# Performance work log

Hardware: AMD Instinct MI355X
Metric: run time of the kernel (lower is better)

## Reference

```python
import jax, jax.numpy as jnp
import numpy as np

N = 50000      # nodes
E = 800000     # edges (before self-loops)
IN_DIM = 128
HID = 64
HEADS = 4
NEG_SLOPE = 0.2  # PyG GATConv default leaky-relu slope


def setup_inputs() -> dict:
    key = jax.random.key(0)
    ks = jax.random.split(key, 12)
    s = 0.05
    return {
        "x": jax.random.normal(ks[0], (N, IN_DIM), jnp.float32),
        "edge_index": jax.random.randint(ks[1], (2, E), 0, N, dtype=jnp.int64),
        "W1": jax.random.normal(ks[2], (IN_DIM, HEADS * HID), jnp.float32) * s,
        "att1_src": jax.random.normal(ks[3], (HEADS, HID), jnp.float32) * s,
        "att1_dst": jax.random.normal(ks[4], (HEADS, HID), jnp.float32) * s,
        "b1": jax.random.normal(ks[5], (HEADS * HID,), jnp.float32) * s,
        "W2": jax.random.normal(ks[6], (HEADS * HID, HID), jnp.float32) * s,
        "att2_src": jax.random.normal(ks[7], (1, HID), jnp.float32) * s,
        "att2_dst": jax.random.normal(ks[8], (1, HID), jnp.float32) * s,
        "b2": jax.random.normal(ks[9], (HID,), jnp.float32) * s,
        "Wc": jax.random.normal(ks[10], (HID, 2), jnp.float32) * s,
        "bc": jax.random.normal(ks[11], (2,), jnp.float32) * s,
    }


def _gat_conv(x, src, dst, W, a_src, a_dst, b, heads, d, concat):
    """PyG GATConv (eval mode): gather-score-segment_softmax-scatter."""
    n = x.shape[0]
    h = (x @ W).reshape(n, heads, d)               # [N,H,D]
    alpha_s = jnp.einsum('nhd,hd->nh', h, a_src)   # [N,H]
    alpha_d = jnp.einsum('nhd,hd->nh', h, a_dst)
    e = jax.nn.leaky_relu(alpha_s[src] + alpha_d[dst], NEG_SLOPE)  # [E,H]
    # softmax over incoming edges of each destination node
    m = jax.ops.segment_max(e, dst, num_segments=n)                # [N,H]
    ex = jnp.exp(e - m[dst])
    den = jax.ops.segment_sum(ex, dst, num_segments=n)
    alpha = ex / den[dst]                                          # [E,H]
    out = jax.ops.segment_sum(h[src] * alpha[:, :, None], dst, num_segments=n)  # [N,H,D]
    out = out.reshape(n, heads * d) if concat else out.mean(axis=1)
    return out + b


def reference(x, edge_index, W1, att1_src, att1_dst, b1,
              W2, att2_src, att2_dst, b2, Wc, bc):
    n = x.shape[0]
    # PyG GATConv adds self-loops by default
    loops = jnp.arange(n, dtype=edge_index.dtype)
    src = jnp.concatenate([edge_index[0], loops])
    dst = jnp.concatenate([edge_index[1], loops])
    h1 = jax.nn.elu(_gat_conv(x, src, dst, W1, att1_src, att1_dst, b1, HEADS, HID, True))
    h2 = jax.nn.elu(_gat_conv(h1, src, dst, W2, att2_src, att2_dst, b2, 1, HID, False))
    return h2 @ Wc + bc
```

## Files before the change

kernel.cpp:

```cpp
#include <hip/hip_runtime.h>
#include <hip/hip_bf16.h>
#include <cstddef>


#define HEADS 4
#define HID 64
#define IN_DIM 128

using bf16x8 = __attribute__((ext_vector_type(8))) short;
using f32x4  = __attribute__((ext_vector_type(4))) float;

__device__ __forceinline__ float us2f(unsigned short u) {
    return __uint_as_float((unsigned int)u << 16);
}
__device__ __forceinline__ unsigned short f2us(float f) {
    __hip_bfloat16 b = __float2bfloat16(f);
    return __builtin_bit_cast(unsigned short, b);
}

__global__ __launch_bounds__(256) void setup_kernel(const float* __restrict__ W1,
                                                    const float* __restrict__ W2,
                                                    unsigned short* __restrict__ W1T,
                                                    unsigned short* __restrict__ W2T,
                                                    int* __restrict__ deg, int N) {
    int i = blockIdx.x * 256 + threadIdx.x;
    if (i < N) deg[i] = 1;
    if (i < IN_DIM * 256) {
        int k = i >> 8, n = i & 255;
        W1T[n * IN_DIM + k] = f2us(W1[i]);
    }
    if (i < 256 * 64) {
        int k = i >> 6, n = i & 63;
        W2T[n * 256 + k] = f2us(W2[i]);
    }
}

template <int BN, int BK, int KFULL, bool INTERLEAVE, bool AF32, int NHEAD>
__global__ __launch_bounds__(256) void gemm_mfma_kernel(
    const void* __restrict__ Av,
    const unsigned short* __restrict__ BT,
    unsigned short* __restrict__ C,
    const float* __restrict__ att_src, const float* __restrict__ att_dst,
    float* __restrict__ as_out, float* __restrict__ ad_out,
    int M, int Nfull) {
    constexpr int LDK = BK + 8;
    constexpr int NT = BN / 16;
    constexpr int KC = BK / 8;
    __shared__ unsigned short As[64 * LDK];
    __shared__ unsigned short Bs[BN * LDK];
    const int tid = threadIdx.x;
    const int wave = tid >> 6, lane = tid & 63;
    const int row0 = blockIdx.y * 64;
    const int col0 = blockIdx.x * BN;
    f32x4 acc[NT] = {};
    for (int k0 = 0; k0 < KFULL; k0 += BK) {
        for (int c = tid; c < 64 * KC; c += 256) {
            int r = c / KC, kc = c - r * KC;
            int row = row0 + r; if (row >= M) row = M - 1;
            if constexpr (AF32) {
                const float* src = (const float*)Av + (size_t)row * KFULL + k0 + kc * 8;
                float4 v0 = *(const float4*)(src);
                float4 v1 = *(const float4*)(src + 4);
                *(ushort4*)(As + r * LDK + kc * 8) =
                    make_ushort4(f2us(v0.x), f2us(v0.y), f2us(v0.z), f2us(v0.w));
                *(ushort4*)(As + r * LDK + kc * 8 + 4) =
                    make_ushort4(f2us(v1.x), f2us(v1.y), f2us(v1.z), f2us(v1.w));
            } else {
                *(bf16x8*)(As + r * LDK + kc * 8) =
                    *(const bf16x8*)((const unsigned short*)Av + (size_t)row * KFULL + k0 + kc * 8);
            }
        }
        for (int c = tid; c < BN * KC; c += 256) {
            int r = c / KC, kc = c - r * KC;
            *(bf16x8*)(Bs + r * LDK + kc * 8) =
                *(const bf16x8*)(BT + (size_t)(col0 + r) * KFULL + k0 + kc * 8);
        }
        __syncthreads();
        const int arow = wave * 16 + (lane & 15);
        const int kb = (lane >> 4) * 8;
#pragma unroll
        for (int ks = 0; ks < BK; ks += 32) {
            bf16x8 af = *(const bf16x8*)(As + arow * LDK + ks + kb);
#pragma unroll
            for (int nt = 0; nt < NT; ++nt) {
                bf16x8 bfv = *(const bf16x8*)(Bs + (nt * 16 + (lane & 15)) * LDK + ks + kb);
                acc[nt] = __builtin_amdgcn_mfma_f32_16x16x32_bf16(af, bfv, acc[nt], 0, 0, 0);
            }
        }
        __syncthreads();
    }
    const int crow0 = row0 + wave * 16 + ((lane >> 4) << 2);
#pragma unroll
    for (int nt = 0; nt < NT; ++nt) {
        const int col = col0 + nt * 16 + (lane & 15);
#pragma unroll
        for (int j = 0; j < 4; ++j) {
            const int row = crow0 + j;
            if (row < M) {
                size_t off = INTERLEAVE
                    ? (size_t)row * 256 + (size_t)(col & 63) * 4 + (col >> 6)
                    : (size_t)row * Nfull + col;
                C[off] = f2us(acc[nt][j]);
            }
        }
    }
    if constexpr (NHEAD > 0) {
        constexpr int NTL = NT / NHEAD;
        float sc[NT], dc[NT];
#pragma unroll
        for (int nt = 0; nt < NT; ++nt) {
            sc[nt] = att_src[nt * 16 + (lane & 15)];
            dc[nt] = att_dst[nt * 16 + (lane & 15)];
        }
#pragma unroll
        for (int j = 0; j < 4; ++j) {
            const int row = crow0 + j;
            float hs[NHEAD], hd[NHEAD];
#pragma unroll
            for (int h = 0; h < NHEAD; ++h) {
                float vs = 0.f, vd = 0.f;
#pragma unroll
                for (int t = 0; t < NTL; ++t) {
                    int nt = h * NTL + t;
                    vs += acc[nt][j] * sc[nt];
                    vd += acc[nt][j] * dc[nt];
                }
#pragma unroll
                for (int off = 1; off < 16; off <<= 1) {
                    vs += __shfl_xor(vs, off, 64);
                    vd += __shfl_xor(vd, off, 64);
                }
                hs[h] = vs; hd[h] = vd;
            }
            if ((lane & 15) == 0 && row < M) {
                if constexpr (NHEAD == 4) {
                    *(float4*)(as_out + (size_t)row * 4) = make_float4(hs[0], hs[1], hs[2], hs[3]);
                    *(float4*)(ad_out + (size_t)row * 4) = make_float4(hd[0], hd[1], hd[2], hd[3]);
                } else {
                    as_out[row] = hs[0];
                    ad_out[row] = hd[0];
                }
            }
        }
    }
}

__global__ void deg_count_kernel(const int* __restrict__ dst, int* __restrict__ deg, int E) {
    int e = blockIdx.x * 256 + threadIdx.x;
    if (e < E) atomicAdd(&deg[dst[e]], 1);
}
__global__ __launch_bounds__(256) void scan1_kernel(const int* __restrict__ deg,
                                                    int* __restrict__ bsum, int N) {
    const int i = blockIdx.x * 256 + threadIdx.x;
    const int lane = threadIdx.x & 63, w = threadIdx.x >> 6;
    int v = (i < N) ? deg[i] : 0;
#pragma unroll
    for (int off = 32; off; off >>= 1) v += __shfl_xor(v, off, 64);
    __shared__ int ws[4];
    if (lane == 0) ws[w] = v;
    __syncthreads();
    if (threadIdx.x == 0) bsum[blockIdx.x] = ws[0] + ws[1] + ws[2] + ws[3];
}
__global__ __launch_bounds__(256) void scan2_kernel(const int* __restrict__ bsum,
                                                    int* __restrict__ boff, int nb) {
    const int tid = threadIdx.x, lane = tid & 63, w = tid >> 6;
    int v = (tid < nb) ? bsum[tid] : 0;
    int x = v;
#pragma unroll
    for (int off = 1; off < 64; off <<= 1) {
        int y = __shfl_up(x, off, 64);
        if (lane >= off) x += y;
    }
    __shared__ int ws[4];
    if (lane == 63) ws[w] = x;
    __syncthreads();
    int add = 0;
    for (int i = 0; i < w; ++i) add += ws[i];
    x += add;
    if (tid < nb) boff[tid] = x - v;
    if (tid == 255) boff[nb] = x;
}
__global__ __launch_bounds__(256) void scan3_kernel(const int* __restrict__ deg,
                                                    const int* __restrict__ boff,
                                                    int* __restrict__ row_ptr,
                                                    int2* __restrict__ edgeA,
                                                    int* __restrict__ fill, int N) {
    const int i = blockIdx.x * 256 + threadIdx.x;
    const int tid = threadIdx.x, lane = tid & 63, w = tid >> 6;
    int v = (i < N) ? deg[i] : 0;
    int x = v;
#pragma unroll
    for (int off = 1; off < 64; off <<= 1) {
        int y = __shfl_up(x, off, 64);
        if (lane >= off) x += y;
    }
    __shared__ int ws[4];
    if (lane == 63) ws[w] = x;
    __syncthreads();
    int add = 0;
    for (int k = 0; k < w; ++k) add += ws[k];
    x += add;
    int excl = x - v + boff[blockIdx.x];
    if (i < N) {
        row_ptr[i] = excl;
        edgeA[excl] = make_int2(i, i);
        fill[i] = excl + 1;
    }
    if (i == N - 1) row_ptr[N] = excl + v;
}
__global__ void scatter_kernel(const int* __restrict__ src, const int* __restrict__ dst,
                               int* __restrict__ fill, int2* __restrict__ edgeA, int E) {
    int e = blockIdx.x * 256 + threadIdx.x;
    if (e < E) {
        int d = dst[e];
        int pos = atomicAdd(&fill[d], 1);
        edgeA[pos] = make_int2(src[e], d);
    }
}

template <int H>
__global__ __launch_bounds__(256) void wkernel(const int2* __restrict__ edgeA,
                                               const float* __restrict__ as,
                                               const float* __restrict__ ad,
                                               float* __restrict__ wA, int NNZ) {
    int p = blockIdx.x * 256 + threadIdx.x;
    if (p >= NNZ) return;
    const int2 e2 = edgeA[p];
    const int src = e2.x, dst = e2.y;
    if constexpr (H == 4) {
        float4 s = *(const float4*)(as + (size_t)src * 4);
        float4 d = *(const float4*)(ad + (size_t)dst * 4);
        float e;
        float4 w;
        e = s.x + d.x; e = e > 0.f ? e : 0.2f * e; w.x = __expf(e);
        e = s.y + d.y; e = e > 0.f ? e : 0.2f * e; w.y = __expf(e);
        e = s.z + d.z; e = e > 0.f ? e : 0.2f * e; w.z = __expf(e);
        e = s.w + d.w; e = e > 0.f ? e : 0.2f * e; w.w = __expf(e);
        *(float4*)(wA + (size_t)p * 4) = w;
    } else {
        float e = as[src] + ad[dst];
        e = e > 0.f ? e : 0.2f * e;
        wA[p] = __expf(e);
    }
}

#define B1 12
__global__ __launch_bounds__(256) void agg1_kernel(
    const unsigned short* __restrict__ g1, const float* __restrict__ wA,
    const int* __restrict__ row_ptr, const int2* __restrict__ edgeA,
    const float* __restrict__ b1, unsigned short* __restrict__ h1b, int N) {
    int wid = (blockIdx.x * 256 + threadIdx.x) >> 6;
    int lane = threadIdx.x & 63;
    if (wid >= N) return;
    float s0 = 0.f, s1 = 0.f, s2 = 0.f, s3 = 0.f;
    float a0 = 0.f, a1 = 0.f, a2 = 0.f, a3 = 0.f;
    const int beg = row_ptr[wid], end = row_ptr[wid + 1];
    for (int idx = beg; idx < end; idx += B1) {
        int p[B1];
#pragma unroll
        for (int j = 0; j < B1; ++j) { int q = idx + j; p[j] = q < end ? q : end - 1; }
        int si[B1];
#pragma unroll
        for (int j = 0; j < B1; ++j) si[j] = edgeA[p[j]].x;
        float4 w[B1];
#pragma unroll
        for (int j = 0; j < B1; ++j) w[j] = *(const float4*)(wA + (size_t)p[j] * 4);
        ushort4 g[B1];
#pragma unroll
        for (int j = 0; j < B1; ++j)
            g[j] = *(const ushort4*)(g1 + ((size_t)si[j] << 8) + lane * 4);
#pragma unroll
        for (int j = 0; j < B1; ++j) {
            const float m = (idx + j < end) ? 1.f : 0.f;
            const float wx = w[j].x * m, wy = w[j].y * m;
            const float wz = w[j].z * m, ww = w[j].w * m;
            s0 += wx; a0 += wx * us2f(g[j].x);
            s1 += wy; a1 += wy * us2f(g[j].y);
            s2 += wz; a2 += wz * us2f(g[j].z);
            s3 += ww; a3 += ww * us2f(g[j].w);
        }
    }
    size_t base = (size_t)wid * 256;
    float o;
    o = a0 / s0 + b1[lane];       o = o > 0.f ? o : expm1f(o); h1b[base + lane]       = f2us(o);
    o = a1 / s1 + b1[64 + lane];  o = o > 0.f ? o : expm1f(o); h1b[base + 64 + lane]  = f2us(o);
    o = a2 / s2 + b1[128 + lane]; o = o > 0.f ? o : expm1f(o); h1b[base + 128 + lane] = f2us(o);
    o = a3 / s3 + b1[192 + lane]; o = o > 0.f ? o : expm1f(o); h1b[base + 192 + lane] = f2us(o);
}

#define B2 32
__global__ __launch_bounds__(256) void agg2_kernel(
    const unsigned short* __restrict__ g2, const float* __restrict__ wA,
    const int* __restrict__ row_ptr, const int2* __restrict__ edgeA,
    const float* __restrict__ b2, const float* __restrict__ Wc,
    const float* __restrict__ bc, float* __restrict__ out, int N) {
    int wid = (blockIdx.x * 256 + threadIdx.x) >> 6;
    int lane = threadIdx.x & 63;
    if (wid >= N) return;
    float s = 0.f, a = 0.f;
    const int beg = row_ptr[wid], end = row_ptr[wid + 1];
    for (int idx = beg; idx < end; idx += B2) {
        int p[B2];
#pragma unroll
        for (int j = 0; j < B2; ++j) { int q = idx + j; p[j] = q < end ? q : end - 1; }
        int si[B2];
#pragma unroll
        for (int j = 0; j < B2; ++j) si[j] = edgeA[p[j]].x;
        float w[B2];
#pragma unroll
        for (int j = 0; j < B2; ++j) w[j] = wA[p[j]];
        unsigned short g[B2];
#pragma unroll
        for (int j = 0; j < B2; ++j) g[j] = g2[((size_t)si[j] << 6) + lane];
#pragma unroll
        for (int j = 0; j < B2; ++j) {
            const float m = (idx + j < end) ? 1.f : 0.f;
            const float wj = w[j] * m;
            s += wj; a += wj * us2f(g[j]);
        }
    }
    float h = a / s + b2[lane];
    h = h > 0.f ? h : expm1f(h);
    float c0 = h * Wc[lane * 2 + 0];
    float c1 = h * Wc[lane * 2 + 1];
#pragma unroll
    for (int off = 32; off; off >>= 1) {
        c0 += __shfl_xor(c0, off, 64);
        c1 += __shfl_xor(c1, off, 64);
    }
    if (lane == 0) {
        out[(size_t)wid * 2 + 0] = c0 + bc[0];
        out[(size_t)wid * 2 + 1] = c1 + bc[1];
    }
}

extern "C" void kernel_launch(void* const* d_in, const int* in_sizes, int n_in,
                              void* d_out, int out_size, void* d_ws, size_t ws_size,
                              hipStream_t stream) {
    const float* x        = (const float*)d_in[0];
    const int*   ei       = (const int*)d_in[1];
    const float* W1       = (const float*)d_in[2];
    const float* att1_src = (const float*)d_in[3];
    const float* att1_dst = (const float*)d_in[4];
    const float* b1       = (const float*)d_in[5];
    const float* W2       = (const float*)d_in[6];
    const float* att2_src = (const float*)d_in[7];
    const float* att2_dst = (const float*)d_in[8];
    const float* b2       = (const float*)d_in[9];
    const float* Wc       = (const float*)d_in[10];
    const float* bc       = (const float*)d_in[11];
    float* out = (float*)d_out;

    const int N = in_sizes[0] / IN_DIM;
    const int E = in_sizes[1] / 2;
    const int NNZ = E + N;
    const int* srcI = ei;
    const int* dstI = ei + E;

    unsigned short* g1b = (unsigned short*)d_ws;
    unsigned short* h1b = g1b + (size_t)N * 256;
    unsigned short* g2b = h1b + (size_t)N * 256;
    unsigned short* W1T = g2b + (size_t)N * 64;
    unsigned short* W2T = W1T + 256 * 128;
    float* as1 = (float*)(W2T + 64 * 256);
    float* ad1 = as1 + (size_t)N * 4;
    float* as2 = ad1 + (size_t)N * 4;
    float* ad2 = as2 + N;
    float* wA1 = ad2 + N;
    float* wA2 = wA1 + (size_t)NNZ * 4;
    int2* edgeA  = (int2*)(wA2 + NNZ);
    int* deg     = (int*)(edgeA + NNZ);
    int* row_ptr = deg + N;
    int* fill    = row_ptr + N + 1;
    int* bsum    = fill + N;
    int* boff    = bsum + 256;

    const int nB = (N + 255) / 256;
    const int eB = (E + 255) / 256;
    const int pB = (NNZ + 255) / 256;
    const int wB = ((N * 64) + 255) / 256;
    const int nb = nB;

    setup_kernel<<<nB, 256, 0, stream>>>(W1, W2, W1T, W2T, deg, N);

    deg_count_kernel<<<eB, 256, 0, stream>>>(dstI, deg, E);
    scan1_kernel<<<nB, 256, 0, stream>>>(deg, bsum, N);
    scan2_kernel<<<1, 256, 0, stream>>>(bsum, boff, nb);
    scan3_kernel<<<nB, 256, 0, stream>>>(deg, boff, row_ptr, edgeA, fill, N);
    scatter_kernel<<<eB, 256, 0, stream>>>(srcI, dstI, fill, edgeA, E);

    gemm_mfma_kernel<256, 64, 128, true, true, 4>
        <<<dim3(1, (N + 63) / 64), 256, 0, stream>>>(x, W1T, g1b,
                                                     att1_src, att1_dst, as1, ad1, N, 256);
    wkernel<4><<<pB, 256, 0, stream>>>(edgeA, as1, ad1, wA1, NNZ);
    agg1_kernel<<<wB, 256, 0, stream>>>(g1b, wA1, row_ptr, edgeA, b1, h1b, N);

    gemm_mfma_kernel<64, 128, 256, false, false, 1>
        <<<dim3(1, (N + 63) / 64), 256, 0, stream>>>(h1b, W2T, g2b,
                                                     att2_src, att2_dst, as2, ad2, N, 64);
    wkernel<1><<<pB, 256, 0, stream>>>(edgeA, as2, ad2, wA2, NNZ);
    agg2_kernel<<<wB, 256, 0, stream>>>(g2b, wA2, row_ptr, edgeA, b2, Wc, bc, out, N);
}
```

Baseline: 400.9 us.

## Split layer-1 aggregation into two head-pair passes with separate feature tables

The first-layer GEMM now writes its output as two tables, each holding two heads interleaved, and the edge-weight kernel writes the matching per-pair weights. Aggregation then runs as two passes, each gathering half-width rows. The goal is a smaller random-gather working set per pass for better cache hit rates. In exchange, edge indices and row pointers are read twice and there is an extra launch. The unroll batch sizes for both aggregation kernels are also reduced.

```diff
diff --git a/kernel.cpp b/kernel.cpp
--- a/kernel.cpp
+++ b/kernel.cpp
@@ -40,6 +40,7 @@
     const void* __restrict__ Av,
     const unsigned short* __restrict__ BT,
     unsigned short* __restrict__ C,
+    unsigned short* __restrict__ C2,
     const float* __restrict__ att_src, const float* __restrict__ att_dst,
     float* __restrict__ as_out, float* __restrict__ ad_out,
     int M, int Nfull) {
@@ -97,10 +98,13 @@
         for (int j = 0; j < 4; ++j) {
             const int row = crow0 + j;
             if (row < M) {
-                size_t off = INTERLEAVE
-                    ? (size_t)row * 256 + (size_t)(col & 63) * 4 + (col >> 6)
-                    : (size_t)row * Nfull + col;
-                C[off] = f2us(acc[nt][j]);
+                if constexpr (INTERLEAVE) {
+                    const int d = col & 63, h = col >> 6;
+                    unsigned short* t = (h & 2) ? C2 : C;
+                    t[(size_t)row * 128 + d * 2 + (h & 1)] = f2us(acc[nt][j]);
+                } else {
+                    C[(size_t)row * Nfull + col] = f2us(acc[nt][j]);
+                }
             }
         }
     }
@@ -222,7 +226,8 @@
 __global__ __launch_bounds__(256) void wkernel(const int2* __restrict__ edgeA,
                                                const float* __restrict__ as,
                                                const float* __restrict__ ad,
-                                               float* __restrict__ wA, int NNZ) {
+                                               float* __restrict__ wA,
+                                               float* __restrict__ wB, int NNZ) {
     int p = blockIdx.x * 256 + threadIdx.x;
     if (p >= NNZ) return;
     const int2 e2 = edgeA[p];
@@ -231,12 +236,13 @@
         float4 s = *(const float4*)(as + (size_t)src * 4);
         float4 d = *(const float4*)(ad + (size_t)dst * 4);
         float e;
-        float4 w;
-        e = s.x + d.x; e = e > 0.f ? e : 0.2f * e; w.x = __expf(e);
-        e = s.y + d.y; e = e > 0.f ? e : 0.2f * e; w.y = __expf(e);
-        e = s.z + d.z; e = e > 0.f ? e : 0.2f * e; w.z = __expf(e);
-        e = s.w + d.w; e = e > 0.f ? e : 0.2f * e; w.w = __expf(e);
-        *(float4*)(wA + (size_t)p * 4) = w;
+        float w0, w1, w2, w3;
+        e = s.x + d.x; e = e > 0.f ? e : 0.2f * e; w0 = __expf(e);
+        e = s.y + d.y; e = e > 0.f ? e : 0.2f * e; w1 = __expf(e);
+        e = s.z + d.z; e = e > 0.f ? e : 0.2f * e; w2 = __expf(e);
+        e = s.w + d.w; e = e > 0.f ? e : 0.2f * e; w3 = __expf(e);
+        *(float2*)(wA + (size_t)p * 2) = make_float2(w0, w1);
+        *(float2*)(wB + (size_t)p * 2) = make_float2(w2, w3);
     } else {
         float e = as[src] + ad[dst];
         e = e > 0.f ? e : 0.2f * e;
@@ -244,16 +250,17 @@
     }
 }
 
-#define B1 12
-__global__ __launch_bounds__(256) void agg1_kernel(
-    const unsigned short* __restrict__ g1, const float* __restrict__ wA,
+#define B1 8
+__global__ __launch_bounds__(256) void agg1_pass_kernel(
+    const unsigned short* __restrict__ tbl,
+    const float* __restrict__ wpair,
     const int* __restrict__ row_ptr, const int2* __restrict__ edgeA,
-    const float* __restrict__ b1, unsigned short* __restrict__ h1b, int N) {
+    const float* __restrict__ b1, unsigned short* __restrict__ h1b,
+    int hoff, int N) {
     int wid = (blockIdx.x * 256 + threadIdx.x) >> 6;
     int lane = threadIdx.x & 63;
     if (wid >= N) return;
-    float s0 = 0.f, s1 = 0.f, s2 = 0.f, s3 = 0.f;
-    float a0 = 0.f, a1 = 0.f, a2 = 0.f, a3 = 0.f;
+    float s0 = 0.f, s1 = 0.f, a0 = 0.f, a1 = 0.f;
     const int beg = row_ptr[wid], end = row_ptr[wid + 1];
     for (int idx = beg; idx < end; idx += B1) {
         int p[B1];
@@ -262,33 +269,30 @@
         int si[B1];
 #pragma unroll
         for (int j = 0; j < B1; ++j) si[j] = edgeA[p[j]].x;
-        float4 w[B1];
-#pragma unroll
-        for (int j = 0; j < B1; ++j) w[j] = *(const float4*)(wA + (size_t)p[j] * 4);
-        ushort4 g[B1];
+        float2 w[B1];
+#pragma unroll
+        for (int j = 0; j < B1; ++j) w[j] = *(const float2*)(wpair + (size_t)p[j] * 2);
+        ushort2 g[B1];
 #pragma unroll
         for (int j = 0; j < B1; ++j)
-            g[j] = *(const ushort4*)(g1 + ((size_t)si[j] << 8) + lane * 4);
+            g[j] = *(const ushort2*)(tbl + ((size_t)si[j] << 7) + lane * 2);
 #pragma unroll
         for (int j = 0; j < B1; ++j) {
             const float m = (idx + j < end) ? 1.f : 0.f;
             const float wx = w[j].x * m, wy = w[j].y * m;
-            const float wz = w[j].z * m, ww = w[j].w * m;
             s0 += wx; a0 += wx * us2f(g[j].x);
             s1 += wy; a1 += wy * us2f(g[j].y);
-            s2 += wz; a2 += wz * us2f(g[j].z);
-            s3 += ww; a3 += ww * us2f(g[j].w);
-        }
-    }
-    size_t base = (size_t)wid * 256;
+        }
+    }
+    size_t base = (size_t)wid * 256 + hoff * 64;
     float o;
-    o = a0 / s0 + b1[lane];       o = o > 0.f ? o : expm1f(o); h1b[base + lane]       = f2us(o);
-    o = a1 / s1 + b1[64 + lane];  o = o > 0.f ? o : expm1f(o); h1b[base + 64 + lane]  = f2us(o);
-    o = a2 / s2 + b1[128 + lane]; o = o > 0.f ? o : expm1f(o); h1b[base + 128 + lane] = f2us(o);
-    o = a3 / s3 + b1[192 + lane]; o = o > 0.f ? o : expm1f(o); h1b[base + 192 + lane] = f2us(o);
-}
-
-#define B2 32
+    o = a0 / s0 + b1[hoff * 64 + lane];
+    o = o > 0.f ? o : expm1f(o); h1b[base + lane] = f2us(o);
+    o = a1 / s1 + b1[hoff * 64 + 64 + lane];
+    o = o > 0.f ? o : expm1f(o); h1b[base + 64 + lane] = f2us(o);
+}
+
+#define B2 16
 __global__ __launch_bounds__(256) void agg2_kernel(
     const unsigned short* __restrict__ g2, const float* __restrict__ wA,
     const int* __restrict__ row_ptr, const int2* __restrict__ edgeA,
@@ -357,17 +361,19 @@
     const int* srcI = ei;
     const int* dstI = ei + E;
 
-    unsigned short* g1b = (unsigned short*)d_ws;
-    unsigned short* h1b = g1b + (size_t)N * 256;
-    unsigned short* g2b = h1b + (size_t)N * 256;
-    unsigned short* W1T = g2b + (size_t)N * 64;
-    unsigned short* W2T = W1T + 256 * 128;
+    unsigned short* g1b0 = (unsigned short*)d_ws;
+    unsigned short* g1b1 = g1b0 + (size_t)N * 128;
+    unsigned short* h1b  = g1b1 + (size_t)N * 128;
+    unsigned short* g2b  = h1b + (size_t)N * 256;
+    unsigned short* W1T  = g2b + (size_t)N * 64;
+    unsigned short* W2T  = W1T + 256 * 128;
     float* as1 = (float*)(W2T + 64 * 256);
     float* ad1 = as1 + (size_t)N * 4;
     float* as2 = ad1 + (size_t)N * 4;
     float* ad2 = as2 + N;
-    float* wA1 = ad2 + N;
-    float* wA2 = wA1 + (size_t)NNZ * 4;
+    float* wA1a = ad2 + N;
+    float* wA1b = wA1a + (size_t)NNZ * 2;
+    float* wA2  = wA1b + (size_t)NNZ * 2;
     int2* edgeA  = (int2*)(wA2 + NNZ);
     int* deg     = (int*)(edgeA + NNZ);
     int* row_ptr = deg + N;
@@ -390,14 +396,15 @@
     scatter_kernel<<<eB, 256, 0, stream>>>(srcI, dstI, fill, edgeA, E);
 
     gemm_mfma_kernel<256, 64, 128, true, true, 4>
-        <<<dim3(1, (N + 63) / 64), 256, 0, stream>>>(x, W1T, g1b,
+        <<<dim3(1, (N + 63) / 64), 256, 0, stream>>>(x, W1T, g1b0, g1b1,
                                                      att1_src, att1_dst, as1, ad1, N, 256);
-    wkernel<4><<<pB, 256, 0, stream>>>(edgeA, as1, ad1, wA1, NNZ);
-    agg1_kernel<<<wB, 256, 0, stream>>>(g1b, wA1, row_ptr, edgeA, b1, h1b, N);
+    wkernel<4><<<pB, 256, 0, stream>>>(edgeA, as1, ad1, wA1a, wA1b, NNZ);
+    agg1_pass_kernel<<<wB, 256, 0, stream>>>(g1b0, wA1a, row_ptr, edgeA, b1, h1b, 0, N);
+    agg1_pass_kernel<<<wB, 256, 0, stream>>>(g1b1, wA1b, row_ptr, edgeA, b1, h1b, 2, N);
 
     gemm_mfma_kernel<64, 128, 256, false, false, 1>
-        <<<dim3(1, (N + 63) / 64), 256, 0, stream>>>(h1b, W2T, g2b,
+        <<<dim3(1, (N + 63) / 64), 256, 0, stream>>>(h1b, W2T, g2b, nullptr,
                                                      att2_src, att2_dst, as2, ad2, N, 64);
-    wkernel<1><<<pB, 256, 0, stream>>>(edgeA, as2, ad2, wA2, NNZ);
+    wkernel<1><<<pB, 256, 0, stream>>>(edgeA, as2, ad2, wA2, nullptr, NNZ);
     agg2_kernel<<<wB, 256, 0, stream>>>(g2b, wA2, row_ptr, edgeA, b2, Wc, bc, out, N);
 }
```

After: 374.6 us. 1.07x faster.
